# Optimization experiments

Measured on AMD Instinct MI355X. Metric: run time of the kernel, lower is better.

The kernel has to match this reference:

```python
import jax, jax.numpy as jnp
import numpy as np

N_NODES = 100000


def gcn_conv(x, W, b, src, dst, n):
    """PyG GCNConv with add_self_loops=True, normalize=True, edge_weight=None.

    Self loops are handled analytically (weight 1 each) instead of appending
    N extra edges: out[i] += deg_inv_sqrt[i]^2 * h[i].
    """
    h = x @ W  # [N, out_dim]
    ones = jnp.ones(src.shape[0], dtype=h.dtype)
    deg = jax.ops.segment_sum(ones, dst, num_segments=n) + 1.0  # +1 self loop
    dis = jnp.where(deg > 0, jax.lax.rsqrt(deg), 0.0)  # deg^{-1/2}
    norm = dis[src] * dis[dst]  # [E]
    agg = jax.ops.segment_sum(h[src] * norm[:, None], dst, num_segments=n)
    agg = agg + h * (dis * dis)[:, None]  # self-loop contribution
    return agg + b


def setup_inputs() -> dict:
    key = jax.random.key(0)
    ks = jax.random.split(key, 6)
    N, E, F, H1, H2, C = N_NODES, 1600000, 500, 128, 64, 10
    x = jax.random.normal(ks[0], (N, F), dtype=jnp.float32)
    edge_index = jax.random.randint(ks[1], (2, E), 0, N, dtype=jnp.int64)
    W1 = jax.random.normal(ks[2], (F, H1), dtype=jnp.float32) * (1.0 / np.sqrt(F))
    b1 = jnp.zeros((H1,), dtype=jnp.float32)
    W2 = jax.random.normal(ks[3], (H1, H2), dtype=jnp.float32) * (1.0 / np.sqrt(H1))
    b2 = jnp.zeros((H2,), dtype=jnp.float32)
    Wc = jax.random.normal(ks[4], (H2, C), dtype=jnp.float32) * (1.0 / np.sqrt(H2))
    bc = jnp.zeros((C,), dtype=jnp.float32)
    return {"x": x, "edge_index": edge_index, "W1": W1, "b1": b1,
            "W2": W2, "b2": b2, "Wc": Wc, "bc": bc}


def reference(x, edge_index, W1, b1, W2, b2, Wc, bc):
    src, dst = edge_index[0], edge_index[1]
    n = x.shape[0]
    h = jax.nn.relu(gcn_conv(x, W1, b1, src, dst, n))
    # dropout is identity at inference (training=False)
    h = jax.nn.relu(gcn_conv(h, W2, b2, src, dst, n))
    return h @ Wc + bc
```

## Files before the change

### kernel.cpp

```cpp
#include <hip/hip_runtime.h>

#define FDIM 500
#define H1DIM 128
#define H2DIM 64
#define CDIM 10

using f32x4 = __attribute__((ext_vector_type(4))) float;
using bf16x8 = __attribute__((ext_vector_type(8))) short;

__device__ __forceinline__ unsigned short f32_to_bf16(float f) {
    unsigned u = __builtin_bit_cast(unsigned, f);
    u += 0x7FFFu + ((u >> 16) & 1u);
    return (unsigned short)(u >> 16);
}
__device__ __forceinline__ float bf16_to_f32(unsigned short h) {
    return __builtin_bit_cast(float, (unsigned)h << 16);
}
__device__ __forceinline__ float blo(unsigned u) {
    return __builtin_bit_cast(float, u << 16);
}
__device__ __forceinline__ float bhi(unsigned u) {
    return __builtin_bit_cast(float, u & 0xFFFF0000u);
}


__global__ __launch_bounds__(256) void hist_kernel(const int* __restrict__ dst,
                                                   int* __restrict__ cnt, int E) {
    int e = blockIdx.x * 256 + threadIdx.x;
    if (e < E) atomicAdd(&cnt[dst[e]], 1);
}

__global__ __launch_bounds__(256) void dis_kernel(const int* __restrict__ cnt,
                                                  float* __restrict__ dis, int n) {
    int i = blockIdx.x * 256 + threadIdx.x;
    if (i < n) dis[i] = rsqrtf((float)cnt[i] + 1.0f);
}

__global__ __launch_bounds__(256) void block_reduce_kernel(const int* __restrict__ cnt,
                                                           int* __restrict__ bsums, int n) {
    __shared__ int s[256];
    int i = blockIdx.x * 256 + threadIdx.x;
    s[threadIdx.x] = (i < n) ? cnt[i] : 0;
    __syncthreads();
    for (int o = 128; o > 0; o >>= 1) {
        if (threadIdx.x < o) s[threadIdx.x] += s[threadIdx.x + o];
        __syncthreads();
    }
    if (threadIdx.x == 0) bsums[blockIdx.x] = s[0];
}

__global__ __launch_bounds__(512) void scan_sums_kernel(int* __restrict__ bsums, int nb,
                                                        int* __restrict__ row_ptr, int n) {
    __shared__ int s[512];
    int v = (threadIdx.x < nb) ? bsums[threadIdx.x] : 0;
    s[threadIdx.x] = v;
    __syncthreads();
    for (int o = 1; o < 512; o <<= 1) {
        int t = (threadIdx.x >= o) ? s[threadIdx.x - o] : 0;
        __syncthreads();
        s[threadIdx.x] += t;
        __syncthreads();
    }
    if (threadIdx.x < nb) bsums[threadIdx.x] = s[threadIdx.x] - v;
    if (threadIdx.x == 511) row_ptr[n] = s[511];
}

__global__ __launch_bounds__(256) void scan_blocks_kernel(const int* __restrict__ cnt,
                                                          const int* __restrict__ bsums,
                                                          int* __restrict__ row_ptr,
                                                          int* __restrict__ cursor, int n) {
    __shared__ int s[256];
    int i = blockIdx.x * 256 + threadIdx.x;
    int v = (i < n) ? cnt[i] : 0;
    s[threadIdx.x] = v;
    __syncthreads();
    for (int o = 1; o < 256; o <<= 1) {
        int t = (threadIdx.x >= o) ? s[threadIdx.x - o] : 0;
        __syncthreads();
        s[threadIdx.x] += t;
        __syncthreads();
    }
    int excl = s[threadIdx.x] - v + bsums[blockIdx.x];
    if (i < n) {
        row_ptr[i] = excl;
        cursor[i] = excl;
    }
}

__global__ __launch_bounds__(256) void fill_kernel(const int* __restrict__ src,
                                                   const int* __restrict__ dst,
                                                   const float* __restrict__ dis,
                                                   int* __restrict__ cursor,
                                                   int2* __restrict__ ew, int E) {
    int e = blockIdx.x * 256 + threadIdx.x;
    if (e < E) {
        int d = dst[e];
        int s = src[e];
        int pos = atomicAdd(&cursor[d], 1);
        float w = dis[s] * dis[d];
        ew[pos] = make_int2(s, __builtin_bit_cast(int, w));
    }
}

__global__ __launch_bounds__(256) void pack_w_kernel(const float* __restrict__ W,
                                                     unsigned short* __restrict__ Bp,
                                                     int K, int N, int T) {
    int idx = blockIdx.x * 256 + threadIdx.x;
    int NF = N >> 4;
    int total = T * NF * 64;
    if (idx >= total) return;
    int lane = idx & 63;
    int tnf = idx >> 6;
    int nf = tnf % NF;
    int t = tnf / NF;
    int kbase = t * 32 + (lane >> 4) * 8;
    int n = nf * 16 + (lane & 15);
    unsigned short v[8];
#pragma unroll
    for (int j = 0; j < 8; j++) {
        int k = kbase + j;
        float f = (k < K) ? W[(size_t)k * N + n] : 0.f;
        v[j] = f32_to_bf16(f);
    }
    uint4 p;
    p.x = (unsigned)v[0] | ((unsigned)v[1] << 16);
    p.y = (unsigned)v[2] | ((unsigned)v[3] << 16);
    p.z = (unsigned)v[4] | ((unsigned)v[5] << 16);
    p.w = (unsigned)v[6] | ((unsigned)v[7] << 16);
    *(uint4*)(Bp + (size_t)idx * 8) = p;
}

template <int NB, int K, bool ABF16>
__global__ __launch_bounds__(64) void gemm_mfma(const void* __restrict__ Avoid,
                                                const unsigned short* __restrict__ Bp,
                                                unsigned short* __restrict__ C, int M) {
    constexpr int NF = NB / 16;
    constexpr int FULL = K / 32;
    constexpr int REM = K % 32;
    const int lane = threadIdx.x;
    const int quad = lane >> 4;
    const int mrow = lane & 15;
    const int m_base = blockIdx.x * 64;

    f32x4 acc[4][NF];
#pragma unroll
    for (int i = 0; i < 4; i++)
#pragma unroll
        for (int j = 0; j < NF; j++) acc[i][j] = (f32x4)(0.f);

    int c[4];
#pragma unroll
    for (int i = 0; i < 4; i++) c[i] = min(m_base + i * 16 + mrow, M - 1);

    const float* Af = (const float*)Avoid;
    const unsigned short* Ah = (const unsigned short*)Avoid;

    for (int t = 0; t < FULL; t++) {
        const int k0 = t * 32 + quad * 8;
        bf16x8 a[4];
        if (ABF16) {
#pragma unroll
            for (int i = 0; i < 4; i++)
                a[i] = *(const bf16x8*)(Ah + (size_t)c[i] * K + k0);
        } else {
#pragma unroll
            for (int i = 0; i < 4; i++) {
                const float* p = Af + (size_t)c[i] * K + k0;
                float4 x = *(const float4*)p, y = *(const float4*)(p + 4);
                a[i][0] = (short)f32_to_bf16(x.x); a[i][1] = (short)f32_to_bf16(x.y);
                a[i][2] = (short)f32_to_bf16(x.z); a[i][3] = (short)f32_to_bf16(x.w);
                a[i][4] = (short)f32_to_bf16(y.x); a[i][5] = (short)f32_to_bf16(y.y);
                a[i][6] = (short)f32_to_bf16(y.z); a[i][7] = (short)f32_to_bf16(y.w);
            }
        }
#pragma unroll
        for (int nf = 0; nf < NF; nf++) {
            bf16x8 b = *(const bf16x8*)(Bp + (size_t)(t * NF + nf) * 512 + lane * 8);
#pragma unroll
            for (int i = 0; i < 4; i++)
                acc[i][nf] = __builtin_amdgcn_mfma_f32_16x16x32_bf16(a[i], b, acc[i][nf], 0, 0, 0);
        }
    }
    if constexpr (REM > 0) {
        const int kb = FULL * 32 + quad * 8;
        bf16x8 a[4];
#pragma unroll
        for (int i = 0; i < 4; i++) {
#pragma unroll
            for (int j = 0; j < 8; j++) {
                int k = kb + j;
                float v = 0.f;
                if (k < K)
                    v = ABF16 ? bf16_to_f32(Ah[(size_t)c[i] * K + k]) : Af[(size_t)c[i] * K + k];
                a[i][j] = (short)f32_to_bf16(v);
            }
        }
#pragma unroll
        for (int nf = 0; nf < NF; nf++) {
            bf16x8 b = *(const bf16x8*)(Bp + (size_t)(FULL * NF + nf) * 512 + lane * 8);
#pragma unroll
            for (int i = 0; i < 4; i++)
                acc[i][nf] = __builtin_amdgcn_mfma_f32_16x16x32_bf16(a[i], b, acc[i][nf], 0, 0, 0);
        }
    }

#pragma unroll
    for (int i = 0; i < 4; i++)
#pragma unroll
        for (int ii = 0; ii < 4; ii++) {
            const int r = m_base + i * 16 + quad * 4 + ii;
            if (r < M) {
#pragma unroll
                for (int nf = 0; nf < NF; nf++)
                    C[(size_t)r * NB + nf * 16 + mrow] = f32_to_bf16(acc[i][nf][ii]);
            }
        }
}

__global__ __launch_bounds__(256) void aggregate128_v3(const uint2* __restrict__ h,
                                                       const float* __restrict__ dis,
                                                       const int* __restrict__ row_ptr,
                                                       const int2* __restrict__ ew,
                                                       const float* __restrict__ bias,
                                                       uint2* __restrict__ out, int n) {
    const int node = blockIdx.x * 4 + (threadIdx.x >> 6);
    if (node >= n) return;
    const int lane = threadIdx.x & 63;
    const int half = lane >> 5;
    const int c = lane & 31;
    const float di = dis[node];
    const int beg = row_ptr[node], end = row_ptr[node + 1];

    float ax0, ax1, ax2, ax3;
    {
        uint2 v = h[(size_t)node * 32 + c];
        float ws = half ? 0.f : di * di;
        ax0 = ws * blo(v.x); ax1 = ws * bhi(v.x);
        ax2 = ws * blo(v.y); ax3 = ws * bhi(v.y);
    }
    for (int jb = beg; jb < end; jb += 16) {
        int2 p[8];
#pragma unroll
        for (int u = 0; u < 8; u++)
            p[u] = ew[min(jb + half + 2 * u, end - 1)];
        float w[8];
        uint2 v[8];
#pragma unroll
        for (int u = 0; u < 8; u++) {
            const bool ok = (jb + half + 2 * u) < end;
            w[u] = ok ? __builtin_bit_cast(float, p[u].y) : 0.f;
            if (ok) v[u] = h[(size_t)p[u].x * 32 + c];
            else    v[u] = make_uint2(0u, 0u);
        }
#pragma unroll
        for (int u = 0; u < 8; u++) {
            ax0 = fmaf(w[u], blo(v[u].x), ax0); ax1 = fmaf(w[u], bhi(v[u].x), ax1);
            ax2 = fmaf(w[u], blo(v[u].y), ax2); ax3 = fmaf(w[u], bhi(v[u].y), ax3);
        }
    }
    ax0 += __shfl_xor(ax0, 32);
    ax1 += __shfl_xor(ax1, 32);
    ax2 += __shfl_xor(ax2, 32);
    ax3 += __shfl_xor(ax3, 32);
    if (half == 0) {
        const float4 b = *(const float4*)(bias + 4 * c);
        uint2 r;
        r.x = (unsigned)f32_to_bf16(fmaxf(ax0 + b.x, 0.f)) |
              ((unsigned)f32_to_bf16(fmaxf(ax1 + b.y, 0.f)) << 16);
        r.y = (unsigned)f32_to_bf16(fmaxf(ax2 + b.z, 0.f)) |
              ((unsigned)f32_to_bf16(fmaxf(ax3 + b.w, 0.f)) << 16);
        out[(size_t)node * 32 + c] = r;
    }
}

__global__ __launch_bounds__(256) void aggregate64_v3(const uint2* __restrict__ h,
                                                      const float* __restrict__ dis,
                                                      const int* __restrict__ row_ptr,
                                                      const int2* __restrict__ ew,
                                                      const float* __restrict__ bias,
                                                      float4* __restrict__ out, int n) {
    const int node = blockIdx.x * 4 + (threadIdx.x >> 6);
    if (node >= n) return;
    const int lane = threadIdx.x & 63;
    const int quad = lane >> 4;
    const int c = lane & 15;
    const float di = dis[node];
    const int beg = row_ptr[node], end = row_ptr[node + 1];

    float ax0, ax1, ax2, ax3;
    {
        uint2 v = h[(size_t)node * 16 + c];
        float ws = quad ? 0.f : di * di;
        ax0 = ws * blo(v.x); ax1 = ws * bhi(v.x);
        ax2 = ws * blo(v.y); ax3 = ws * bhi(v.y);
    }
    for (int jb = beg; jb < end; jb += 16) {
        int2 p[4];
#pragma unroll
        for (int u = 0; u < 4; u++)
            p[u] = ew[min(jb + quad + 4 * u, end - 1)];
        float w[4];
        uint2 v[4];
#pragma unroll
        for (int u = 0; u < 4; u++) {
            const bool ok = (jb + quad + 4 * u) < end;
            w[u] = ok ? __builtin_bit_cast(float, p[u].y) : 0.f;
            if (ok) v[u] = h[(size_t)p[u].x * 16 + c];
            else    v[u] = make_uint2(0u, 0u);
        }
#pragma unroll
        for (int u = 0; u < 4; u++) {
            ax0 = fmaf(w[u], blo(v[u].x), ax0); ax1 = fmaf(w[u], bhi(v[u].x), ax1);
            ax2 = fmaf(w[u], blo(v[u].y), ax2); ax3 = fmaf(w[u], bhi(v[u].y), ax3);
        }
    }
    ax0 += __shfl_xor(ax0, 16); ax0 += __shfl_xor(ax0, 32);
    ax1 += __shfl_xor(ax1, 16); ax1 += __shfl_xor(ax1, 32);
    ax2 += __shfl_xor(ax2, 16); ax2 += __shfl_xor(ax2, 32);
    ax3 += __shfl_xor(ax3, 16); ax3 += __shfl_xor(ax3, 32);
    if (lane < 16) {
        const float4 b = *(const float4*)(bias + 4 * c);
        float4 r;
        r.x = fmaxf(ax0 + b.x, 0.f);
        r.y = fmaxf(ax1 + b.y, 0.f);
        r.z = fmaxf(ax2 + b.z, 0.f);
        r.w = fmaxf(ax3 + b.w, 0.f);
        out[(size_t)node * 16 + c] = r;
    }
}

__global__ __launch_bounds__(256) void classifier_kernel(const float* __restrict__ A,
                                                         const float* __restrict__ Wc,
                                                         const float* __restrict__ bc,
                                                         float* __restrict__ out, int M) {
    int idx = blockIdx.x * 256 + threadIdx.x;
    int row = idx >> 4;
    int c = idx & 15;
    if (row >= M || c >= CDIM) return;
    const float* a = A + (size_t)row * H2DIM;
    float acc = bc[c];
#pragma unroll 8
    for (int k = 0; k < H2DIM; k++) acc = fmaf(a[k], Wc[k * CDIM + c], acc);
    out[(size_t)row * CDIM + c] = acc;
}


extern "C" void kernel_launch(void* const* d_in, const int* in_sizes, int n_in,
                              void* d_out, int out_size, void* d_ws, size_t ws_size,
                              hipStream_t stream) {
    const float* x  = (const float*)d_in[0];
    const int*   ei = (const int*)d_in[1];
    const float* W1 = (const float*)d_in[2];
    const float* b1 = (const float*)d_in[3];
    const float* W2 = (const float*)d_in[4];
    const float* b2 = (const float*)d_in[5];
    const float* Wc = (const float*)d_in[6];
    const float* bc = (const float*)d_in[7];
    float* out = (float*)d_out;

    const int N = in_sizes[0] / FDIM;
    const int E = in_sizes[1] / 2;
    const int* src = ei;
    const int* dst = ei + E;

    char* ws = (char*)d_ws;
    int*            cnt    = (int*)(ws + 0x000000);
    int*            rowptr = (int*)(ws + 0x080000);
    float*          dis    = (float*)(ws + 0x100000);
    int*            bsums  = (int*)(ws + 0x180000);
    int2*           ew     = (int2*)(ws + 0x200000);
    unsigned short* W1p    = (unsigned short*)(ws + 0xE40000);
    unsigned short* W2p    = (unsigned short*)(ws + 0xE80000);
    unsigned short* h1     = (unsigned short*)(ws + 0xF00000);
    float*          agg2f  = (float*)(ws + 0xF00000);
    unsigned short* agg1   = (unsigned short*)(ws + 0x2800000);
    unsigned short* h2     = (unsigned short*)(ws + 0x4200000);

    const int nb = (N + 255) / 256;

    hipMemsetAsync(cnt, 0, (size_t)N * sizeof(int), stream);
    hist_kernel<<<(E + 255) / 256, 256, 0, stream>>>(dst, cnt, E);
    dis_kernel<<<nb, 256, 0, stream>>>(cnt, dis, N);
    block_reduce_kernel<<<nb, 256, 0, stream>>>(cnt, bsums, N);
    scan_sums_kernel<<<1, 512, 0, stream>>>(bsums, nb, rowptr, N);
    scan_blocks_kernel<<<nb, 256, 0, stream>>>(cnt, bsums, rowptr, cnt, N);
    fill_kernel<<<(E + 255) / 256, 256, 0, stream>>>(src, dst, dis, cnt, ew, E);

    pack_w_kernel<<<(16 * 8 * 64 + 255) / 256, 256, 0, stream>>>(W1, W1p, FDIM, H1DIM, 16);
    pack_w_kernel<<<(4 * 4 * 64 + 255) / 256, 256, 0, stream>>>(W2, W2p, H1DIM, H2DIM, 4);

    const int gblocks = (N + 63) / 64;

    gemm_mfma<H1DIM, FDIM, false><<<gblocks, 64, 0, stream>>>(x, W1p, h1, N);
    aggregate128_v3<<<(N + 3) / 4, 256, 0, stream>>>((const uint2*)h1, dis, rowptr, ew, b1,
                                                     (uint2*)agg1, N);
    gemm_mfma<H2DIM, H1DIM, true><<<gblocks, 64, 0, stream>>>(agg1, W2p, h2, N);
    aggregate64_v3<<<(N + 3) / 4, 256, 0, stream>>>((const uint2*)h2, dis, rowptr, ew, b2,
                                                    (float4*)agg2f, N);

    classifier_kernel<<<(N * 16 + 255) / 256, 256, 0, stream>>>(agg2f, Wc, bc, out, N);
}
```

Before: 624.4 us.

## Store GEMM outputs in feature-chunked layout and aggregate per 16-column chunk

The GEMMs now write hidden features as 16-column chunks stored contiguously per chunk across all nodes. Aggregation launches one grid slice per chunk, so each slice's gathers touch a smaller working set (n*32 bytes) that can stay in L2/MALL cache. Each wave handles two nodes with 8 edges in parallel and 4 lanes per node row. The cost is re-reading the edge list once per chunk (8x and 4x), plus shorter 32-byte gathers.

```diff
diff --git a/kernel.cpp b/kernel.cpp
--- a/kernel.cpp
+++ b/kernel.cpp
@@ -130,7 +130,7 @@
     *(uint4*)(Bp + (size_t)idx * 8) = p;
 }
 
-template <int NB, int K, bool ABF16>
+template <int NB, int K, bool ABF16, bool CHUNKED>
 __global__ __launch_bounds__(64) void gemm_mfma(const void* __restrict__ Avoid,
                                                 const unsigned short* __restrict__ Bp,
                                                 unsigned short* __restrict__ C, int M) {
@@ -211,121 +211,75 @@
             const int r = m_base + i * 16 + quad * 4 + ii;
             if (r < M) {
 #pragma unroll
-                for (int nf = 0; nf < NF; nf++)
-                    C[(size_t)r * NB + nf * 16 + mrow] = f32_to_bf16(acc[i][nf][ii]);
+                for (int nf = 0; nf < NF; nf++) {
+                    const size_t idx = CHUNKED ? ((size_t)nf * M + r) * 16 + mrow
+                                               : (size_t)r * NB + nf * 16 + mrow;
+                    C[idx] = f32_to_bf16(acc[i][nf][ii]);
+                }
             }
         }
 }
 
-__global__ __launch_bounds__(256) void aggregate128_v3(const uint2* __restrict__ h,
-                                                       const float* __restrict__ dis,
-                                                       const int* __restrict__ row_ptr,
-                                                       const int2* __restrict__ ew,
-                                                       const float* __restrict__ bias,
-                                                       uint2* __restrict__ out, int n) {
-    const int node = blockIdx.x * 4 + (threadIdx.x >> 6);
-    if (node >= n) return;
+template <int D, bool OUTBF16>
+__global__ __launch_bounds__(256) void aggregate_chunked(const uint2* __restrict__ hc,
+                                                         const float* __restrict__ dis,
+                                                         const int* __restrict__ row_ptr,
+                                                         const int2* __restrict__ ew,
+                                                         const float* __restrict__ bias,
+                                                         void* __restrict__ outv, int n) {
     const int lane = threadIdx.x & 63;
-    const int half = lane >> 5;
-    const int c = lane & 31;
-    const float di = dis[node];
-    const int beg = row_ptr[node], end = row_ptr[node + 1];
+    const int wid = threadIdx.x >> 6;
+    const int nsub = lane >> 5;
+    const int eslot = (lane >> 2) & 7;
+    const int cpos = lane & 3;
+    const int node = (blockIdx.x * 4 + wid) * 2 + nsub;
+    const bool active = node < n;
+    const int nc = active ? node : n - 1;
+    const int ch = blockIdx.y;
+    const uint2* slice = hc + (size_t)ch * n * 4;
+
+    const float di = dis[nc];
+    const int beg = row_ptr[nc];
+    const int end = active ? row_ptr[nc + 1] : beg;
 
     float ax0, ax1, ax2, ax3;
     {
-        uint2 v = h[(size_t)node * 32 + c];
-        float ws = half ? 0.f : di * di;
+        uint2 v = slice[(size_t)nc * 4 + cpos];
+        float ws = (eslot == 0) ? di * di : 0.f;
         ax0 = ws * blo(v.x); ax1 = ws * bhi(v.x);
         ax2 = ws * blo(v.y); ax3 = ws * bhi(v.y);
     }
-    for (int jb = beg; jb < end; jb += 16) {
-        int2 p[8];
-#pragma unroll
-        for (int u = 0; u < 8; u++)
-            p[u] = ew[min(jb + half + 2 * u, end - 1)];
-        float w[8];
-        uint2 v[8];
-#pragma unroll
-        for (int u = 0; u < 8; u++) {
-            const bool ok = (jb + half + 2 * u) < end;
-            w[u] = ok ? __builtin_bit_cast(float, p[u].y) : 0.f;
-            if (ok) v[u] = h[(size_t)p[u].x * 32 + c];
-            else    v[u] = make_uint2(0u, 0u);
-        }
-#pragma unroll
-        for (int u = 0; u < 8; u++) {
-            ax0 = fmaf(w[u], blo(v[u].x), ax0); ax1 = fmaf(w[u], bhi(v[u].x), ax1);
-            ax2 = fmaf(w[u], blo(v[u].y), ax2); ax3 = fmaf(w[u], bhi(v[u].y), ax3);
-        }
-    }
-    ax0 += __shfl_xor(ax0, 32);
-    ax1 += __shfl_xor(ax1, 32);
-    ax2 += __shfl_xor(ax2, 32);
-    ax3 += __shfl_xor(ax3, 32);
-    if (half == 0) {
-        const float4 b = *(const float4*)(bias + 4 * c);
-        uint2 r;
-        r.x = (unsigned)f32_to_bf16(fmaxf(ax0 + b.x, 0.f)) |
-              ((unsigned)f32_to_bf16(fmaxf(ax1 + b.y, 0.f)) << 16);
-        r.y = (unsigned)f32_to_bf16(fmaxf(ax2 + b.z, 0.f)) |
-              ((unsigned)f32_to_bf16(fmaxf(ax3 + b.w, 0.f)) << 16);
-        out[(size_t)node * 32 + c] = r;
-    }
-}
-
-__global__ __launch_bounds__(256) void aggregate64_v3(const uint2* __restrict__ h,
-                                                      const float* __restrict__ dis,
-                                                      const int* __restrict__ row_ptr,
-                                                      const int2* __restrict__ ew,
-                                                      const float* __restrict__ bias,
-                                                      float4* __restrict__ out, int n) {
-    const int node = blockIdx.x * 4 + (threadIdx.x >> 6);
-    if (node >= n) return;
-    const int lane = threadIdx.x & 63;
-    const int quad = lane >> 4;
-    const int c = lane & 15;
-    const float di = dis[node];
-    const int beg = row_ptr[node], end = row_ptr[node + 1];
-
-    float ax0, ax1, ax2, ax3;
-    {
-        uint2 v = h[(size_t)node * 16 + c];
-        float ws = quad ? 0.f : di * di;
-        ax0 = ws * blo(v.x); ax1 = ws * bhi(v.x);
-        ax2 = ws * blo(v.y); ax3 = ws * bhi(v.y);
-    }
-    for (int jb = beg; jb < end; jb += 16) {
-        int2 p[4];
-#pragma unroll
-        for (int u = 0; u < 4; u++)
-            p[u] = ew[min(jb + quad + 4 * u, end - 1)];
-        float w[4];
-        uint2 v[4];
-#pragma unroll
-        for (int u = 0; u < 4; u++) {
-            const bool ok = (jb + quad + 4 * u) < end;
-            w[u] = ok ? __builtin_bit_cast(float, p[u].y) : 0.f;
-            if (ok) v[u] = h[(size_t)p[u].x * 16 + c];
-            else    v[u] = make_uint2(0u, 0u);
-        }
-#pragma unroll
-        for (int u = 0; u < 4; u++) {
-            ax0 = fmaf(w[u], blo(v[u].x), ax0); ax1 = fmaf(w[u], bhi(v[u].x), ax1);
-            ax2 = fmaf(w[u], blo(v[u].y), ax2); ax3 = fmaf(w[u], bhi(v[u].y), ax3);
-        }
-    }
-    ax0 += __shfl_xor(ax0, 16); ax0 += __shfl_xor(ax0, 32);
-    ax1 += __shfl_xor(ax1, 16); ax1 += __shfl_xor(ax1, 32);
-    ax2 += __shfl_xor(ax2, 16); ax2 += __shfl_xor(ax2, 32);
-    ax3 += __shfl_xor(ax3, 16); ax3 += __shfl_xor(ax3, 32);
-    if (lane < 16) {
-        const float4 b = *(const float4*)(bias + 4 * c);
-        float4 r;
-        r.x = fmaxf(ax0 + b.x, 0.f);
-        r.y = fmaxf(ax1 + b.y, 0.f);
-        r.z = fmaxf(ax2 + b.z, 0.f);
-        r.w = fmaxf(ax3 + b.w, 0.f);
-        out[(size_t)node * 16 + c] = r;
+    for (int jb = beg; jb < end; jb += 8) {
+        const int e = jb + eslot;
+        const bool ok = e < end;
+        long long pe = __builtin_nontemporal_load((const long long*)ew + min(e, end - 1));
+        const int s = (int)(unsigned)pe;
+        const float w = ok ? __builtin_bit_cast(float, (int)(pe >> 32)) : 0.f;
+        uint2 v = make_uint2(0u, 0u);
+        if (ok) v = slice[(size_t)s * 4 + cpos];
+        ax0 = fmaf(w, blo(v.x), ax0); ax1 = fmaf(w, bhi(v.x), ax1);
+        ax2 = fmaf(w, blo(v.y), ax2); ax3 = fmaf(w, bhi(v.y), ax3);
+    }
+    ax0 += __shfl_xor(ax0, 4); ax0 += __shfl_xor(ax0, 8); ax0 += __shfl_xor(ax0, 16);
+    ax1 += __shfl_xor(ax1, 4); ax1 += __shfl_xor(ax1, 8); ax1 += __shfl_xor(ax1, 16);
+    ax2 += __shfl_xor(ax2, 4); ax2 += __shfl_xor(ax2, 8); ax2 += __shfl_xor(ax2, 16);
+    ax3 += __shfl_xor(ax3, 4); ax3 += __shfl_xor(ax3, 8); ax3 += __shfl_xor(ax3, 16);
+    if (eslot == 0 && active) {
+        const float4 b = *(const float4*)(bias + ch * 16 + cpos * 4);
+        const float r0 = fmaxf(ax0 + b.x, 0.f);
+        const float r1 = fmaxf(ax1 + b.y, 0.f);
+        const float r2 = fmaxf(ax2 + b.z, 0.f);
+        const float r3 = fmaxf(ax3 + b.w, 0.f);
+        if (OUTBF16) {
+            uint2 r;
+            r.x = (unsigned)f32_to_bf16(r0) | ((unsigned)f32_to_bf16(r1) << 16);
+            r.y = (unsigned)f32_to_bf16(r2) | ((unsigned)f32_to_bf16(r3) << 16);
+            ((uint2*)outv)[(size_t)node * (D / 4) + ch * 4 + cpos] = r;
+        } else {
+            float4 r;
+            r.x = r0; r.y = r1; r.z = r2; r.w = r3;
+            ((float4*)outv)[(size_t)node * (D / 4) + ch * 4 + cpos] = r;
+        }
     }
 }
 
@@ -390,13 +344,15 @@
     pack_w_kernel<<<(4 * 4 * 64 + 255) / 256, 256, 0, stream>>>(W2, W2p, H1DIM, H2DIM, 4);
 
     const int gblocks = (N + 63) / 64;
-
-    gemm_mfma<H1DIM, FDIM, false><<<gblocks, 64, 0, stream>>>(x, W1p, h1, N);
-    aggregate128_v3<<<(N + 3) / 4, 256, 0, stream>>>((const uint2*)h1, dis, rowptr, ew, b1,
-                                                     (uint2*)agg1, N);
-    gemm_mfma<H2DIM, H1DIM, true><<<gblocks, 64, 0, stream>>>(agg1, W2p, h2, N);
-    aggregate64_v3<<<(N + 3) / 4, 256, 0, stream>>>((const uint2*)h2, dis, rowptr, ew, b2,
-                                                    (float4*)agg2f, N);
+    const int ablocks = (N + 7) / 8;
+
+    gemm_mfma<H1DIM, FDIM, false, true><<<gblocks, 64, 0, stream>>>(x, W1p, h1, N);
+    aggregate_chunked<H1DIM, true><<<dim3(ablocks, H1DIM / 16), 256, 0, stream>>>(
+        (const uint2*)h1, dis, rowptr, ew, b1, agg1, N);
+
+    gemm_mfma<H2DIM, H1DIM, true, true><<<gblocks, 64, 0, stream>>>(agg1, W2p, h2, N);
+    aggregate_chunked<H2DIM, false><<<dim3(ablocks, H2DIM / 16), 256, 0, stream>>>(
+        (const uint2*)h2, dis, rowptr, ew, b2, agg2f, N);
 
     classifier_kernel<<<(N * 16 + 255) / 256, 256, 0, stream>>>(agg2f, Wc, bc, out, N);
 }
```

Result: slower. 854.0 us (+36.8%).

## Split GEMM1 K across four waves and fuse classifier into final aggregation

Applied to the files above, without the earlier changes.

Replaces the single-wave first GEMM with a 256-thread kernel where each wave handles a quarter of the K tiles and partial results are reduced through shared-memory atomics before bf16 store. The classifier matmul is fused into the second aggregation kernel via shared memory, removing the fp32 intermediate buffer and a launch. The deg^-1/2 computation is folded into the scan kernel. The K-split adds LDS atomic reduction overhead and a 32KB shared buffer per block, which may limit occupancy.

```diff
diff --git a/kernel.cpp b/kernel.cpp
--- a/kernel.cpp
+++ b/kernel.cpp
@@ -28,12 +28,6 @@
                                                    int* __restrict__ cnt, int E) {
     int e = blockIdx.x * 256 + threadIdx.x;
     if (e < E) atomicAdd(&cnt[dst[e]], 1);
-}
-
-__global__ __launch_bounds__(256) void dis_kernel(const int* __restrict__ cnt,
-                                                  float* __restrict__ dis, int n) {
-    int i = blockIdx.x * 256 + threadIdx.x;
-    if (i < n) dis[i] = rsqrtf((float)cnt[i] + 1.0f);
 }
 
 __global__ __launch_bounds__(256) void block_reduce_kernel(const int* __restrict__ cnt,
@@ -68,7 +62,8 @@
 __global__ __launch_bounds__(256) void scan_blocks_kernel(const int* __restrict__ cnt,
                                                           const int* __restrict__ bsums,
                                                           int* __restrict__ row_ptr,
-                                                          int* __restrict__ cursor, int n) {
+                                                          int* __restrict__ cursor,
+                                                          float* __restrict__ dis, int n) {
     __shared__ int s[256];
     int i = blockIdx.x * 256 + threadIdx.x;
     int v = (i < n) ? cnt[i] : 0;
@@ -84,6 +79,7 @@
     if (i < n) {
         row_ptr[i] = excl;
         cursor[i] = excl;
+        dis[i] = rsqrtf((float)v + 1.0f);
     }
 }
 
@@ -130,6 +126,101 @@
     *(uint4*)(Bp + (size_t)idx * 8) = p;
 }
 
+template <int NB, int K>
+__global__ __launch_bounds__(256) void gemm1_ksplit(const float* __restrict__ Af,
+                                                    const unsigned short* __restrict__ Bp,
+                                                    unsigned short* __restrict__ C, int M) {
+    constexpr int NF = NB / 16;
+    constexpr int TILES = (K + 31) / 32;
+    constexpr int FULL = K / 32;
+    const int tid = threadIdx.x;
+    const int w = tid >> 6;
+    const int lane = tid & 63;
+    const int quad = lane >> 4;
+    const int mrow = lane & 15;
+    const int m_base = blockIdx.x * 64;
+
+    __shared__ float red[64 * NB];
+    for (int i = tid; i < 64 * NB; i += 256) red[i] = 0.f;
+
+    f32x4 acc[4][NF];
+#pragma unroll
+    for (int i = 0; i < 4; i++)
+#pragma unroll
+        for (int j = 0; j < NF; j++) acc[i][j] = (f32x4)(0.f);
+
+    int c[4];
+#pragma unroll
+    for (int i = 0; i < 4; i++) c[i] = min(m_base + i * 16 + mrow, M - 1);
+
+    const int t0 = w * (TILES / 4);
+    const int t1 = t0 + TILES / 4;
+    __syncthreads();
+
+    for (int t = t0; t < t1; t++) {
+        const int k0 = t * 32 + quad * 8;
+        bf16x8 a[4];
+        if (t < FULL) {
+#pragma unroll
+            for (int i = 0; i < 4; i++) {
+                const float* p = Af + (size_t)c[i] * K + k0;
+                float4 x = *(const float4*)p, y = *(const float4*)(p + 4);
+                a[i][0] = (short)f32_to_bf16(x.x); a[i][1] = (short)f32_to_bf16(x.y);
+                a[i][2] = (short)f32_to_bf16(x.z); a[i][3] = (short)f32_to_bf16(x.w);
+                a[i][4] = (short)f32_to_bf16(y.x); a[i][5] = (short)f32_to_bf16(y.y);
+                a[i][6] = (short)f32_to_bf16(y.z); a[i][7] = (short)f32_to_bf16(y.w);
+            }
+        } else {
+#pragma unroll
+            for (int i = 0; i < 4; i++) {
+#pragma unroll
+                for (int j = 0; j < 8; j++) {
+                    int k = k0 + j;
+                    float v = (k < K) ? Af[(size_t)c[i] * K + k] : 0.f;
+                    a[i][j] = (short)f32_to_bf16(v);
+                }
+            }
+        }
+#pragma unroll
+        for (int nf = 0; nf < NF; nf++) {
+            bf16x8 b = *(const bf16x8*)(Bp + (size_t)(t * NF + nf) * 512 + lane * 8);
+#pragma unroll
+            for (int i = 0; i < 4; i++)
+                acc[i][nf] = __builtin_amdgcn_mfma_f32_16x16x32_bf16(a[i], b, acc[i][nf], 0, 0, 0);
+        }
+    }
+
+#pragma unroll
+    for (int i = 0; i < 4; i++)
+#pragma unroll
+        for (int ii = 0; ii < 4; ii++) {
+            const int rl = i * 16 + quad * 4 + ii;
+#pragma unroll
+            for (int nf = 0; nf < NF; nf++)
+                atomicAdd(&red[rl * NB + nf * 16 + mrow], acc[i][nf][ii]);
+        }
+    __syncthreads();
+
+    constexpr int GPR = NB / 8;
+    for (int g = tid; g < 64 * GPR; g += 256) {
+        const int row = g / GPR;
+        const int c8 = (g % GPR) * 8;
+        const int r = m_base + row;
+        if (r < M) {
+            const float* src = red + row * NB + c8;
+            unsigned short v[8];
+#pragma unroll
+            for (int j = 0; j < 8; j++) v[j] = f32_to_bf16(src[j]);
+            uint4 p;
+            p.x = (unsigned)v[0] | ((unsigned)v[1] << 16);
+            p.y = (unsigned)v[2] | ((unsigned)v[3] << 16);
+            p.z = (unsigned)v[4] | ((unsigned)v[5] << 16);
+            p.w = (unsigned)v[6] | ((unsigned)v[7] << 16);
+            *(uint4*)(C + (size_t)r * NB + c8) = p;
+        }
+    }
+}
+
 template <int NB, int K, bool ABF16>
 __global__ __launch_bounds__(64) void gemm_mfma(const void* __restrict__ Avoid,
                                                 const unsigned short* __restrict__ Bp,
@@ -273,23 +364,29 @@
     }
 }
 
-__global__ __launch_bounds__(256) void aggregate64_v3(const uint2* __restrict__ h,
-                                                      const float* __restrict__ dis,
-                                                      const int* __restrict__ row_ptr,
-                                                      const int2* __restrict__ ew,
-                                                      const float* __restrict__ bias,
-                                                      float4* __restrict__ out, int n) {
-    const int node = blockIdx.x * 4 + (threadIdx.x >> 6);
-    if (node >= n) return;
+__global__ __launch_bounds__(256) void aggregate64_cls(const uint2* __restrict__ h,
+                                                       const float* __restrict__ dis,
+                                                       const int* __restrict__ row_ptr,
+                                                       const int2* __restrict__ ew,
+                                                       const float* __restrict__ bias,
+                                                       const float* __restrict__ Wc,
+                                                       const float* __restrict__ bc,
+                                                       float* __restrict__ out, int n) {
+    __shared__ float sm[4][H2DIM];
+    const int wid = threadIdx.x >> 6;
     const int lane = threadIdx.x & 63;
     const int quad = lane >> 4;
     const int c = lane & 15;
-    const float di = dis[node];
-    const int beg = row_ptr[node], end = row_ptr[node + 1];
+    const int node = blockIdx.x * 4 + wid;
+    const bool active = node < n;
+    const int nc = active ? node : n - 1;
+    const float di = dis[nc];
+    const int beg = row_ptr[nc];
+    const int end = active ? row_ptr[nc + 1] : beg;
 
     float ax0, ax1, ax2, ax3;
     {
-        uint2 v = h[(size_t)node * 16 + c];
+        uint2 v = h[(size_t)nc * 16 + c];
         float ws = quad ? 0.f : di * di;
         ax0 = ws * blo(v.x); ax1 = ws * bhi(v.x);
         ax2 = ws * blo(v.y); ax3 = ws * bhi(v.y);
@@ -320,28 +417,18 @@
     ax3 += __shfl_xor(ax3, 16); ax3 += __shfl_xor(ax3, 32);
     if (lane < 16) {
         const float4 b = *(const float4*)(bias + 4 * c);
-        float4 r;
-        r.x = fmaxf(ax0 + b.x, 0.f);
-        r.y = fmaxf(ax1 + b.y, 0.f);
-        r.z = fmaxf(ax2 + b.z, 0.f);
-        r.w = fmaxf(ax3 + b.w, 0.f);
-        out[(size_t)node * 16 + c] = r;
-    }
-}
-
-__global__ __launch_bounds__(256) void classifier_kernel(const float* __restrict__ A,
-                                                         const float* __restrict__ Wc,
-                                                         const float* __restrict__ bc,
-                                                         float* __restrict__ out, int M) {
-    int idx = blockIdx.x * 256 + threadIdx.x;
-    int row = idx >> 4;
-    int c = idx & 15;
-    if (row >= M || c >= CDIM) return;
-    const float* a = A + (size_t)row * H2DIM;
-    float acc = bc[c];
+        sm[wid][4 * c + 0] = fmaxf(ax0 + b.x, 0.f);
+        sm[wid][4 * c + 1] = fmaxf(ax1 + b.y, 0.f);
+        sm[wid][4 * c + 2] = fmaxf(ax2 + b.z, 0.f);
+        sm[wid][4 * c + 3] = fmaxf(ax3 + b.w, 0.f);
+    }
+    __syncthreads();
+    if (active && lane < CDIM) {
+        float a2 = bc[lane];
 #pragma unroll 8
-    for (int k = 0; k < H2DIM; k++) acc = fmaf(a[k], Wc[k * CDIM + c], acc);
-    out[(size_t)row * CDIM + c] = acc;
+        for (int k = 0; k < H2DIM; k++) a2 = fmaf(sm[wid][k], Wc[k * CDIM + lane], a2);
+        out[(size_t)node * CDIM + lane] = a2;
+    }
 }
 
 
@@ -372,7 +459,6 @@
     unsigned short* W1p    = (unsigned short*)(ws + 0xE40000);
     unsigned short* W2p    = (unsigned short*)(ws + 0xE80000);
     unsigned short* h1     = (unsigned short*)(ws + 0xF00000);
-    float*          agg2f  = (float*)(ws + 0xF00000);
     unsigned short* agg1   = (unsigned short*)(ws + 0x2800000);
     unsigned short* h2     = (unsigned short*)(ws + 0x4200000);
 
@@ -380,10 +466,9 @@
 
     hipMemsetAsync(cnt, 0, (size_t)N * sizeof(int), stream);
     hist_kernel<<<(E + 255) / 256, 256, 0, stream>>>(dst, cnt, E);
-    dis_kernel<<<nb, 256, 0, stream>>>(cnt, dis, N);
     block_reduce_kernel<<<nb, 256, 0, stream>>>(cnt, bsums, N);
     scan_sums_kernel<<<1, 512, 0, stream>>>(bsums, nb, rowptr, N);
-    scan_blocks_kernel<<<nb, 256, 0, stream>>>(cnt, bsums, rowptr, cnt, N);
+    scan_blocks_kernel<<<nb, 256, 0, stream>>>(cnt, bsums, rowptr, cnt, dis, N);
     fill_kernel<<<(E + 255) / 256, 256, 0, stream>>>(src, dst, dis, cnt, ew, E);
 
     pack_w_kernel<<<(16 * 8 * 64 + 255) / 256, 256, 0, stream>>>(W1, W1p, FDIM, H1DIM, 16);
@@ -391,12 +476,10 @@
 
     const int gblocks = (N + 63) / 64;
 
-    gemm_mfma<H1DIM, FDIM, false><<<gblocks, 64, 0, stream>>>(x, W1p, h1, N);
+    gemm1_ksplit<H1DIM, FDIM><<<gblocks, 256, 0, stream>>>(x, W1p, h1, N);
     aggregate128_v3<<<(N + 3) / 4, 256, 0, stream>>>((const uint2*)h1, dis, rowptr, ew, b1,
                                                      (uint2*)agg1, N);
     gemm_mfma<H2DIM, H1DIM, true><<<gblocks, 64, 0, stream>>>(agg1, W2p, h2, N);
-    aggregate64_v3<<<(N + 3) / 4, 256, 0, stream>>>((const uint2*)h2, dis, rowptr, ew, b2,
-                                                    (float4*)agg2f, N);
-
-    classifier_kernel<<<(N * 16 + 255) / 256, 256, 0, stream>>>(agg2f, Wc, bc, out, N);
-}
+    aggregate64_cls<<<(N + 3) / 4, 256, 0, stream>>>((const uint2*)h2, dis, rowptr, ew, b2,
+                                                     Wc, bc, out, N);
+}
```

After: 928.7 us. 48.7% more time.
